# Kernel optimization log

Measured on AMD Instinct MI355X. Metric: run time of the kernel, lower is better.

## Reference

```python
import jax, jax.numpy as jnp
import numpy as np

WIDTH = 768
HEAD = 64

def setup_inputs() -> dict:
    key = jax.random.key(0)
    ks = jax.random.split(key, 8)
    x = jax.random.normal(ks[0], (8, 2048, WIDTH), dtype=jnp.float32)
    mask = jax.random.randint(ks[1], (2048, 2048), 0, 2, dtype=jnp.int32)
    s = 1.0 / np.sqrt(WIDTH)
    Wq = jax.random.normal(ks[2], (WIDTH, HEAD), dtype=jnp.float32) * s
    Wk = jax.random.normal(ks[3], (WIDTH, HEAD), dtype=jnp.float32) * s
    Wv = jax.random.normal(ks[4], (WIDTH, HEAD), dtype=jnp.float32) * s
    bq = jax.random.normal(ks[5], (HEAD,), dtype=jnp.float32) * 0.01
    bk = jax.random.normal(ks[6], (HEAD,), dtype=jnp.float32) * 0.01
    bv = jax.random.normal(ks[7], (HEAD,), dtype=jnp.float32) * 0.01
    return {"x": x, "Wq": Wq, "bq": bq, "Wk": Wk, "bk": bk, "Wv": Wv, "bv": bv, "mask": mask}

def reference(x, Wq, bq, Wk, bk, Wv, bv, mask) -> jnp.ndarray:
    # x: [B, N, width]; projections -> [B, N, head]
    Q = jnp.einsum('bnw,wh->bnh', x, Wq) + bq
    K = jnp.einsum('bnw,wh->bnh', x, Wk) + bk
    V = jnp.einsum('bnw,wh->bnh', x, Wv) + bv
    scale = 1.0 / jnp.sqrt(jnp.asarray(Q.shape[-1], dtype=Q.dtype))
    scores = jnp.einsum('bqh,bkh->bqk', Q, K) * scale  # [B, N, N]
    scores = jnp.where(mask == 0, -jnp.inf, scores)
    attn = jax.nn.softmax(scores, axis=-1)
    return jnp.einsum('bqk,bkh->bqh', attn, V)
```

## Files before the change

kernel.cpp:

```cpp
#include <hip/hip_runtime.h>

typedef short  s8v   __attribute__((ext_vector_type(8)));
typedef float  f32x4 __attribute__((ext_vector_type(4)));

#define SEQ 2048
#define WID 768

__device__ __forceinline__ unsigned fbits(float f) {
    union { float f; unsigned u; } v; v.f = f; return v.u;
}
__device__ __forceinline__ float bitsf(unsigned u) {
    union { unsigned u; float f; } v; v.u = u; return v.f;
}
__device__ __forceinline__ unsigned short f2b(float f) {
    unsigned u = fbits(f);
    return (unsigned short)((u + 0x7FFFu + ((u >> 16) & 1u)) >> 16);
}
__device__ __forceinline__ unsigned packRNE(float a, float b) {
    unsigned ta = fbits(a) + 0x7FFFu + ((fbits(a) >> 16) & 1u);
    unsigned tb = fbits(b) + 0x7FFFu + ((fbits(b) >> 16) & 1u);
    return __builtin_amdgcn_perm(tb, ta, 0x07060302u);
}
__device__ __forceinline__ unsigned packTRUNC(float a, float b) {
    return __builtin_amdgcn_perm(fbits(b), fbits(a), 0x07060302u);
}
__device__ __forceinline__ f32x4 zero4() { f32x4 z = {0.f, 0.f, 0.f, 0.f}; return z; }

__device__ __forceinline__ void async16(const unsigned short* g, void* l) {
    __builtin_amdgcn_global_load_lds(
        (const __attribute__((address_space(1))) unsigned int*)g,
        (__attribute__((address_space(3))) unsigned int*)l, 16, 0, 0);
}
__device__ __forceinline__ void async16f(const float* g, void* l) {
    __builtin_amdgcn_global_load_lds(
        (const __attribute__((address_space(1))) unsigned int*)g,
        (__attribute__((address_space(3))) unsigned int*)l, 16, 0, 0);
}
__device__ __forceinline__ void async4(const unsigned* g, void* l) {
    __builtin_amdgcn_global_load_lds(
        (const __attribute__((address_space(1))) unsigned int*)g,
        (__attribute__((address_space(3))) unsigned int*)l, 4, 0, 0);
}

__global__ __launch_bounds__(256) void convert_mask_kernel(
    const int* __restrict__ mask, unsigned* __restrict__ PM)
{
    const int tid = threadIdx.x;
    const int gid  = blockIdx.x * 4 + (tid >> 6);
    const int lane = tid & 63, quad = lane >> 4, c = lane & 15;
    const int qb = gid >> 5, kb = gid & 31;
    unsigned w = 0;
    #pragma unroll
    for (int mt = 0; mt < 2; ++mt)
        #pragma unroll
        for (int i = 0; i < 4; ++i) {
            const int q = qb * 32 + mt * 16 + quad * 4 + i;
            const int4 mm = *(const int4*)&mask[(size_t)q * SEQ + kb * 64 + 4 * c];
            if (mm.x) w |= 1u << (mt * 16 + i * 4 + 0);
            if (mm.y) w |= 1u << (mt * 16 + i * 4 + 1);
            if (mm.z) w |= 1u << (mt * 16 + i * 4 + 2);
            if (mm.w) w |= 1u << (mt * 16 + i * 4 + 3);
        }
    PM[(size_t)gid * 64 + lane] = w;
}

__global__ __launch_bounds__(256) void convert_w_kernel(
    const float* __restrict__ Wq, const float* __restrict__ Wk, const float* __restrict__ Wv,
    unsigned short* __restrict__ WF)
{
    const int s2 = blockIdx.x * 256 + threadIdx.x;
    const int chunk = s2 >> 6, l = s2 & 63;
    const int ntg = chunk / 24, r = chunk - ntg * 24;
    const int kc = r >> 1, h = r & 1;
    const int mat = ntg >> 2;
    const int col = (ntg & 3) * 16 + (l & 15);
    const int k0 = kc * 64 + h * 32 + (l >> 4) * 8;
    const float* Wm = (mat == 0) ? Wq : (mat == 1) ? Wk : Wv;
    float p[8];
    #pragma unroll
    for (int j = 0; j < 8; ++j) p[j] = Wm[(size_t)(k0 + j) * 64 + col];
    uint4 w;
    w.x = packRNE(p[0], p[1]); w.y = packRNE(p[2], p[3]);
    w.z = packRNE(p[4], p[5]); w.w = packRNE(p[6], p[7]);
    *(uint4*)&WF[(size_t)s2 * 8] = w;
}

__global__ __launch_bounds__(256, 4) void qkv_proj_kernel(
    const float* __restrict__ x, const unsigned short* __restrict__ WF,
    const float* __restrict__ bq, const float* __restrict__ bk, const float* __restrict__ bv,
    unsigned short* __restrict__ QF, unsigned short* __restrict__ KF,
    unsigned short* __restrict__ VF)
{
    __shared__ __align__(16) unsigned char SM[32768];
    unsigned short (*St)[200] = (unsigned short(*)[200])SM;

    const int tid = threadIdx.x;
    const int wv = tid >> 6, lane = tid & 63, quad = lane >> 4, c = lane & 15;
    const int cg = wv;
    const int rowb = blockIdx.x * 32;

    float bias[3];
    #pragma unroll
    for (int nt = 0; nt < 3; ++nt) {
        int col = cg * 48 + nt * 16 + c;
        const float* B = (col < 64) ? bq : (col < 128) ? bk : bv;
        bias[nt] = B[col & 63];
    }

    auto issue = [&](int kc, int b) {
        unsigned char* base = SM + b * 16384;
        #pragma unroll
        for (int r = 0; r < 4; ++r) {
            const int t = wv * 4 + r;
            if (t < 4) {
                const int mt = t >> 1, jh = t & 1;
                const float* src = x + (size_t)(rowb + mt * 16 + c) * WID
                                     + kc * 32 + quad * 8 + jh * 4;
                async16f(src, base + (mt * 2 + jh) * 1024);
            } else {
                const int i = t - 4;
                const unsigned short* src =
                    WF + (((size_t)i * 12 + (kc >> 1)) * 2 + (kc & 1)) * 512 + lane * 8;
                async16(src, base + 4096 + i * 1024);
            }
        }
    };

    f32x4 acc[2][3];
    #pragma unroll
    for (int mt = 0; mt < 2; ++mt)
        #pragma unroll
        for (int nt = 0; nt < 3; ++nt) acc[mt][nt] = zero4();

    issue(0, 0);
    for (int kc = 0; kc < 24; ++kc) {
        const int b = kc & 1;
        __syncthreads();
        if (kc < 23) issue(kc + 1, b ^ 1);

        const unsigned char* base = SM + b * 16384;
        s8v af[2];
        #pragma unroll
        for (int mt = 0; mt < 2; ++mt) {
            float4 f0 = *(const float4*)(base + (mt * 2 + 0) * 1024 + lane * 16);
            float4 f1 = *(const float4*)(base + (mt * 2 + 1) * 1024 + lane * 16);
            union { uint4 u; s8v v; } a;
            a.u.x = packRNE(f0.x, f0.y);
            a.u.y = packRNE(f0.z, f0.w);
            a.u.z = packRNE(f1.x, f1.y);
            a.u.w = packRNE(f1.z, f1.w);
            af[mt] = a.v;
        }
        s8v bf[3];
        #pragma unroll
        for (int nt = 0; nt < 3; ++nt)
            bf[nt] = *(const s8v*)(base + 4096 + (cg * 3 + nt) * 1024 + lane * 16);
        #pragma unroll
        for (int mt = 0; mt < 2; ++mt)
            #pragma unroll
            for (int nt = 0; nt < 3; ++nt)
                acc[mt][nt] = __builtin_amdgcn_mfma_f32_16x16x32_bf16(
                    af[mt], bf[nt], acc[mt][nt], 0, 0, 0);
    }

    __syncthreads();
    #pragma unroll
    for (int mt = 0; mt < 2; ++mt)
        #pragma unroll
        for (int nt = 0; nt < 3; ++nt)
            #pragma unroll
            for (int i = 0; i < 4; ++i)
                St[mt * 16 + quad * 4 + i][cg * 48 + nt * 16 + c]
                    = f2b(acc[mt][nt][i] + bias[nt]);
    __syncthreads();

    const int kb  = rowb >> 6;
    const int q0k = (rowb & 63) >> 2;
    const int ks0 = (rowb & 63) >> 5;

    {
        const int g = tid >> 7, ks = (tid >> 6) & 1, l = tid & 63;
        uint4 v = *(uint4*)&St[g * 16 + (l & 15)][ks * 32 + (l >> 4) * 8];
        *(uint4*)&QF[(((size_t)(rowb >> 4) + g) * 2 + ks) * 512 + (size_t)l * 8] = v;
    }
    {
        const int ksnt = tid >> 5, e = tid & 31;
        const int ks = ksnt >> 2, nt = ksnt & 3;
        const int qd = e >> 3, cc = e & 7;
        uint4 v = *(uint4*)&St[4 * cc + nt][64 + ks * 32 + qd * 8];
        *(uint4*)&KF[(((size_t)kb * 8 + ksnt) * 64 + qd * 16 + q0k + cc) * 8] = v;
    }
    {
        const int nt = tid >> 6, qd = (tid >> 4) & 3, cc = tid & 15;
        unsigned short p[8];
        #pragma unroll
        for (int s = 0; s < 8; ++s) p[s] = St[qd * 8 + s][128 + nt * 16 + cc];
        uint4 w;
        w.x = (unsigned)p[0] | ((unsigned)p[1] << 16);
        w.y = (unsigned)p[2] | ((unsigned)p[3] << 16);
        w.z = (unsigned)p[4] | ((unsigned)p[5] << 16);
        w.w = (unsigned)p[6] | ((unsigned)p[7] << 16);
        *(uint4*)&VF[(((size_t)kb * 8 + ks0 * 4 + nt) * 64 + qd * 16 + cc) * 8] = w;
    }
}

__global__ __launch_bounds__(512, 4) void attn_kernel(
    const unsigned short* __restrict__ QF, const unsigned short* __restrict__ KF,
    const unsigned short* __restrict__ VF, const unsigned* __restrict__ PM,
    float* __restrict__ out)
{
    __shared__ unsigned short Ks[4][4096];
    __shared__ unsigned PMs[4][64];
    __shared__ __align__(16) unsigned char PsOb[17408];
    __shared__ float Lbuf[32];
    unsigned short (*Ps)[16][68] = (unsigned short(*)[16][68])PsOb;
    float (*Obuf)[68]            = (float(*)[68])PsOb;

    const int tid = threadIdx.x;
    const int wv = tid >> 6, lane = tid & 63, quad = lane >> 4, c = lane & 15;
    const int sl = wv & 3, qh = wv >> 2;
    const int blk = blockIdx.x;
    const int bb = blk & 7, qt = blk >> 3;
    const int qrow_blk = qt * 32;

    s8v qf[2];
    {
        const size_t qgrp = (size_t)bb * 128 + qt * 2 + qh;
        #pragma unroll
        for (int ks = 0; ks < 2; ++ks)
            qf[ks] = *(const s8v*)&QF[(qgrp * 2 + ks) * 512 + (size_t)lane * 8];
    }

    f32x4 O[4];
    float lro[4];
    #pragma unroll
    for (int nt = 0; nt < 4; ++nt) O[nt] = zero4();
    #pragma unroll
    for (int i = 0; i < 4; ++i) lro[i] = 0.f;

    auto k_dma = [&](int kt) {
        const size_t kbg = (size_t)bb * 32 + sl * 8 + kt;
        #pragma unroll
        for (int r = 0; r < 4; ++r) {
            const int ch = qh * 4 + r;
            async16(KF + (kbg * 8 + ch) * 512 + lane * 8, &Ks[sl][ch * 512]);
        }
        if (qh == 0)
            async4(PM + ((size_t)qt * 32 + sl * 8 + kt) * 64 + lane, &PMs[sl][0]);
    };

    k_dma(0);
    for (int kt = 0; kt < 8; ++kt) {
        const size_t kbg = (size_t)bb * 32 + sl * 8 + kt;

        __syncthreads();

        f32x4 S[4];
        #pragma unroll
        for (int nt = 0; nt < 4; ++nt) S[nt] = zero4();
        #pragma unroll
        for (int ks = 0; ks < 2; ++ks) {
            s8v kfr[4];
            #pragma unroll
            for (int nt = 0; nt < 4; ++nt)
                kfr[nt] = *(const s8v*)&Ks[sl][((ks * 4 + nt) * 64 + lane) * 8];
            #pragma unroll
            for (int nt = 0; nt < 4; ++nt)
                S[nt] = __builtin_amdgcn_mfma_f32_16x16x32_bf16(qf[ks], kfr[nt], S[nt], 0, 0, 0);
        }

        const unsigned pmh = PMs[sl][lane] >> (qh * 16);
        #pragma unroll
        for (int i = 0; i < 4; ++i) {
            float p4[4];
            #pragma unroll
            for (int nt = 0; nt < 4; ++nt) {
                float e = exp2f(fmaf(S[nt][i], 0.18033688011112042f, -21.640425613334451f));
                p4[nt] = ((pmh >> (i * 4 + nt)) & 1u) ? e : 0.f;
            }
            unsigned u0 = packTRUNC(p4[0], p4[1]);
            unsigned u1 = packTRUNC(p4[2], p4[3]);
            lro[i] += bitsf(u0 << 16) + bitsf(u0 & 0xFFFF0000u)
                    + bitsf(u1 << 16) + bitsf(u1 & 0xFFFF0000u);
            *(uint2*)&Ps[wv][quad * 4 + i][4 * c] = make_uint2(u0, u1);
        }

        #pragma unroll
        for (int ks = 0; ks < 2; ++ks) {
            s8v vf4[4];
            #pragma unroll
            for (int nt = 0; nt < 4; ++nt)
                vf4[nt] = *(const s8v*)&VF[(kbg * 8 + ks * 4 + nt) * 512 + (size_t)lane * 8];
            s8v a = *(const s8v*)&Ps[wv][c][ks * 32 + quad * 8];
            #pragma unroll
            for (int nt = 0; nt < 4; ++nt)
                O[nt] = __builtin_amdgcn_mfma_f32_16x16x32_bf16(a, vf4[nt], O[nt], 0, 0, 0);
        }

        __syncthreads();
        if (kt < 7) k_dma(kt + 1);
    }

    __syncthreads();
    #pragma unroll
    for (int j = 0; j < 5; ++j) {
        int idx = tid + 512 * j;
        if (idx < 32 * 68) ((float*)Obuf)[idx] = 0.f;
    }
    if (tid < 32) Lbuf[tid] = 0.f;
    __syncthreads();
    #pragma unroll
    for (int i = 0; i < 4; ++i) {
        float l = lro[i];
        l += __shfl_xor(l, 1);
        l += __shfl_xor(l, 2);
        l += __shfl_xor(l, 4);
        l += __shfl_xor(l, 8);
        if (c == 0) atomicAdd(&Lbuf[qh * 16 + quad * 4 + i], l);
        #pragma unroll
        for (int nt = 0; nt < 4; ++nt)
            atomicAdd(&Obuf[qh * 16 + quad * 4 + i][nt * 16 + c], O[nt][i]);
    }
    __syncthreads();
    {
        const int r = tid >> 4, d4 = (tid & 15) * 4;
        const float invL = 1.0f / Lbuf[r];
        float4 v = *(float4*)&Obuf[r][d4];
        float4 o = make_float4(v.x * invL, v.y * invL, v.z * invL, v.w * invL);
        *(float4*)&out[((size_t)bb * SEQ + qrow_blk + r) * 64 + d4] = o;
    }
}

extern "C" void kernel_launch(void* const* d_in, const int* in_sizes, int n_in,
                              void* d_out, int out_size, void* d_ws, size_t ws_size,
                              hipStream_t stream)
{
    const float* x    = (const float*)d_in[0];
    const float* Wq   = (const float*)d_in[1];
    const float* bq   = (const float*)d_in[2];
    const float* Wk   = (const float*)d_in[3];
    const float* bk   = (const float*)d_in[4];
    const float* Wv   = (const float*)d_in[5];
    const float* bv   = (const float*)d_in[6];
    const int*   mask = (const int*)d_in[7];
    float* out = (float*)d_out;

    unsigned short* QF = (unsigned short*)d_ws;
    unsigned short* KF = QF + (size_t)16384 * 64;
    unsigned short* VF = KF + (size_t)16384 * 64;
    unsigned short* WF = VF + (size_t)16384 * 64;
    unsigned*       PM = (unsigned*)(WF + (size_t)192 * WID);

    convert_mask_kernel<<<512, 256, 0, stream>>>(mask, PM);
    convert_w_kernel<<<72, 256, 0, stream>>>(Wq, Wk, Wv, WF);
    qkv_proj_kernel<<<512, 256, 0, stream>>>(x, WF, bq, bk, bv, QF, KF, VF);
    attn_kernel<<<512, 512, 0, stream>>>(QF, KF, VF, PM, out);
}
```

Baseline: 174.0 us.

## Fuse convert kernels, widen QKV k-chunks, double-buffer K tiles in 64-row attention blocks

Merges the mask and weight conversion kernels into one launch. Doubles the per-stage k-chunk in the QKV projection, halving its barrier count at the cost of more shared memory and a lower occupancy bound. Restructures attention into 1024-thread blocks covering 64 query rows, with double-buffered K/mask DMA so the next tile loads while the current one is computed, removing a barrier per iteration. The larger blocks halve the grid and raise shared-memory use per block.

```diff
diff --git a/kernel.cpp b/kernel.cpp
--- a/kernel.cpp
+++ b/kernel.cpp
@@ -42,56 +42,56 @@
         (__attribute__((address_space(3))) unsigned int*)l, 4, 0, 0);
 }
 
-__global__ __launch_bounds__(256) void convert_mask_kernel(
-    const int* __restrict__ mask, unsigned* __restrict__ PM)
+__global__ __launch_bounds__(256) void convert_kernel(
+    const int* __restrict__ mask,
+    const float* __restrict__ Wq, const float* __restrict__ Wk, const float* __restrict__ Wv,
+    unsigned* __restrict__ PM, unsigned short* __restrict__ WF)
 {
     const int tid = threadIdx.x;
-    const int gid  = blockIdx.x * 4 + (tid >> 6);
-    const int lane = tid & 63, quad = lane >> 4, c = lane & 15;
-    const int qb = gid >> 5, kb = gid & 31;
-    unsigned w = 0;
-    #pragma unroll
-    for (int mt = 0; mt < 2; ++mt)
-        #pragma unroll
-        for (int i = 0; i < 4; ++i) {
-            const int q = qb * 32 + mt * 16 + quad * 4 + i;
-            const int4 mm = *(const int4*)&mask[(size_t)q * SEQ + kb * 64 + 4 * c];
-            if (mm.x) w |= 1u << (mt * 16 + i * 4 + 0);
-            if (mm.y) w |= 1u << (mt * 16 + i * 4 + 1);
-            if (mm.z) w |= 1u << (mt * 16 + i * 4 + 2);
-            if (mm.w) w |= 1u << (mt * 16 + i * 4 + 3);
-        }
-    PM[(size_t)gid * 64 + lane] = w;
-}
-
-__global__ __launch_bounds__(256) void convert_w_kernel(
-    const float* __restrict__ Wq, const float* __restrict__ Wk, const float* __restrict__ Wv,
-    unsigned short* __restrict__ WF)
-{
-    const int s2 = blockIdx.x * 256 + threadIdx.x;
-    const int chunk = s2 >> 6, l = s2 & 63;
-    const int ntg = chunk / 24, r = chunk - ntg * 24;
-    const int kc = r >> 1, h = r & 1;
-    const int mat = ntg >> 2;
-    const int col = (ntg & 3) * 16 + (l & 15);
-    const int k0 = kc * 64 + h * 32 + (l >> 4) * 8;
-    const float* Wm = (mat == 0) ? Wq : (mat == 1) ? Wk : Wv;
-    float p[8];
-    #pragma unroll
-    for (int j = 0; j < 8; ++j) p[j] = Wm[(size_t)(k0 + j) * 64 + col];
-    uint4 w;
-    w.x = packRNE(p[0], p[1]); w.y = packRNE(p[2], p[3]);
-    w.z = packRNE(p[4], p[5]); w.w = packRNE(p[6], p[7]);
-    *(uint4*)&WF[(size_t)s2 * 8] = w;
-}
-
-__global__ __launch_bounds__(256, 4) void qkv_proj_kernel(
+    const int blk = blockIdx.x;
+    if (blk < 512) {
+        const int gid  = blk * 4 + (tid >> 6);
+        const int lane = tid & 63, quad = lane >> 4, c = lane & 15;
+        const int qb = gid >> 5, kb = gid & 31;
+        unsigned w = 0;
+        #pragma unroll
+        for (int mt = 0; mt < 2; ++mt)
+            #pragma unroll
+            for (int i = 0; i < 4; ++i) {
+                const int q = qb * 32 + mt * 16 + quad * 4 + i;
+                const int4 mm = *(const int4*)&mask[(size_t)q * SEQ + kb * 64 + 4 * c];
+                if (mm.x) w |= 1u << (mt * 16 + i * 4 + 0);
+                if (mm.y) w |= 1u << (mt * 16 + i * 4 + 1);
+                if (mm.z) w |= 1u << (mt * 16 + i * 4 + 2);
+                if (mm.w) w |= 1u << (mt * 16 + i * 4 + 3);
+            }
+        PM[(size_t)gid * 64 + lane] = w;
+    } else {
+        const int s2 = (blk - 512) * 256 + tid;
+        const int chunk = s2 >> 6, l = s2 & 63;
+        const int ntg = chunk / 24, r = chunk - ntg * 24;
+        const int kc = r >> 1, h = r & 1;
+        const int mat = ntg >> 2;
+        const int col = (ntg & 3) * 16 + (l & 15);
+        const int k0 = kc * 64 + h * 32 + (l >> 4) * 8;
+        const float* Wm = (mat == 0) ? Wq : (mat == 1) ? Wk : Wv;
+        float p[8];
+        #pragma unroll
+        for (int j = 0; j < 8; ++j) p[j] = Wm[(size_t)(k0 + j) * 64 + col];
+        uint4 w;
+        w.x = packRNE(p[0], p[1]); w.y = packRNE(p[2], p[3]);
+        w.z = packRNE(p[4], p[5]); w.w = packRNE(p[6], p[7]);
+        *(uint4*)&WF[(size_t)s2 * 8] = w;
+    }
+}
+
+__global__ __launch_bounds__(256, 2) void qkv_proj_kernel(
     const float* __restrict__ x, const unsigned short* __restrict__ WF,
     const float* __restrict__ bq, const float* __restrict__ bk, const float* __restrict__ bv,
     unsigned short* __restrict__ QF, unsigned short* __restrict__ KF,
     unsigned short* __restrict__ VF)
 {
-    __shared__ __align__(16) unsigned char SM[32768];
+    __shared__ __align__(16) unsigned char SM[65536];
     unsigned short (*St)[200] = (unsigned short(*)[200])SM;
 
     const int tid = threadIdx.x;
@@ -108,20 +108,20 @@
     }
 
     auto issue = [&](int kc, int b) {
-        unsigned char* base = SM + b * 16384;
-        #pragma unroll
-        for (int r = 0; r < 4; ++r) {
-            const int t = wv * 4 + r;
-            if (t < 4) {
-                const int mt = t >> 1, jh = t & 1;
-                const float* src = x + (size_t)(rowb + mt * 16 + c) * WID
-                                     + kc * 32 + quad * 8 + jh * 4;
-                async16f(src, base + (mt * 2 + jh) * 1024);
+        unsigned char* base = SM + b * 32768;
+        #pragma unroll
+        for (int r = 0; r < 8; ++r) {
+            const int t = wv * 8 + r;
+            if (t < 8) {
+                const int g = t >> 2, kh = (t >> 1) & 1, jh = t & 1;
+                const float* src = x + (size_t)(rowb + g * 16 + c) * WID
+                                     + kc * 64 + kh * 32 + quad * 8 + jh * 4;
+                async16f(src, base + t * 1024);
             } else {
-                const int i = t - 4;
+                const int i = t - 8, ntg = i >> 1, kh = i & 1;
                 const unsigned short* src =
-                    WF + (((size_t)i * 12 + (kc >> 1)) * 2 + (kc & 1)) * 512 + lane * 8;
-                async16(src, base + 4096 + i * 1024);
+                    WF + (((size_t)ntg * 12 + kc) * 2 + kh) * 512 + lane * 8;
+                async16(src, base + 8192 + i * 1024);
             }
         }
     };
@@ -133,34 +133,37 @@
         for (int nt = 0; nt < 3; ++nt) acc[mt][nt] = zero4();
 
     issue(0, 0);
-    for (int kc = 0; kc < 24; ++kc) {
+    for (int kc = 0; kc < 12; ++kc) {
         const int b = kc & 1;
         __syncthreads();
-        if (kc < 23) issue(kc + 1, b ^ 1);
-
-        const unsigned char* base = SM + b * 16384;
-        s8v af[2];
-        #pragma unroll
-        for (int mt = 0; mt < 2; ++mt) {
-            float4 f0 = *(const float4*)(base + (mt * 2 + 0) * 1024 + lane * 16);
-            float4 f1 = *(const float4*)(base + (mt * 2 + 1) * 1024 + lane * 16);
-            union { uint4 u; s8v v; } a;
-            a.u.x = packRNE(f0.x, f0.y);
-            a.u.y = packRNE(f0.z, f0.w);
-            a.u.z = packRNE(f1.x, f1.y);
-            a.u.w = packRNE(f1.z, f1.w);
-            af[mt] = a.v;
-        }
-        s8v bf[3];
-        #pragma unroll
-        for (int nt = 0; nt < 3; ++nt)
-            bf[nt] = *(const s8v*)(base + 4096 + (cg * 3 + nt) * 1024 + lane * 16);
-        #pragma unroll
-        for (int mt = 0; mt < 2; ++mt)
+        if (kc < 11) issue(kc + 1, b ^ 1);
+
+        const unsigned char* base = SM + b * 32768;
+        #pragma unroll
+        for (int kh = 0; kh < 2; ++kh) {
+            s8v af[2];
+            #pragma unroll
+            for (int mt = 0; mt < 2; ++mt) {
+                float4 f0 = *(const float4*)(base + (mt * 4 + kh * 2 + 0) * 1024 + lane * 16);
+                float4 f1 = *(const float4*)(base + (mt * 4 + kh * 2 + 1) * 1024 + lane * 16);
+                union { uint4 u; s8v v; } a;
+                a.u.x = packRNE(f0.x, f0.y);
+                a.u.y = packRNE(f0.z, f0.w);
+                a.u.z = packRNE(f1.x, f1.y);
+                a.u.w = packRNE(f1.z, f1.w);
+                af[mt] = a.v;
+            }
+            s8v bf[3];
             #pragma unroll
             for (int nt = 0; nt < 3; ++nt)
-                acc[mt][nt] = __builtin_amdgcn_mfma_f32_16x16x32_bf16(
-                    af[mt], bf[nt], acc[mt][nt], 0, 0, 0);
+                bf[nt] = *(const s8v*)(base + 8192 + ((cg * 3 + nt) * 2 + kh) * 1024 + lane * 16);
+            #pragma unroll
+            for (int mt = 0; mt < 2; ++mt)
+                #pragma unroll
+                for (int nt = 0; nt < 3; ++nt)
+                    acc[mt][nt] = __builtin_amdgcn_mfma_f32_16x16x32_bf16(
+                        af[mt], bf[nt], acc[mt][nt], 0, 0, 0);
+        }
     }
 
     __syncthreads();
@@ -204,28 +207,27 @@
     }
 }
 
-__global__ __launch_bounds__(512, 4) void attn_kernel(
+__global__ __launch_bounds__(1024, 4) void attn_kernel(
     const unsigned short* __restrict__ QF, const unsigned short* __restrict__ KF,
     const unsigned short* __restrict__ VF, const unsigned* __restrict__ PM,
     float* __restrict__ out)
 {
-    __shared__ unsigned short Ks[4][4096];
-    __shared__ unsigned PMs[4][64];
-    __shared__ __align__(16) unsigned char PsOb[17408];
-    __shared__ float Lbuf[32];
+    __shared__ unsigned short Ks[2][4][4096];
+    __shared__ unsigned PMs[2][2][4][64];
+    __shared__ __align__(16) unsigned char PsOb[34816];
+    __shared__ float Lbuf[64];
     unsigned short (*Ps)[16][68] = (unsigned short(*)[16][68])PsOb;
     float (*Obuf)[68]            = (float(*)[68])PsOb;
 
     const int tid = threadIdx.x;
     const int wv = tid >> 6, lane = tid & 63, quad = lane >> 4, c = lane & 15;
-    const int sl = wv & 3, qh = wv >> 2;
+    const int sl = wv & 3, qg = wv >> 2, mt = qg & 1;
     const int blk = blockIdx.x;
     const int bb = blk & 7, qt = blk >> 3;
-    const int qrow_blk = qt * 32;
 
     s8v qf[2];
     {
-        const size_t qgrp = (size_t)bb * 128 + qt * 2 + qh;
+        const size_t qgrp = (size_t)bb * 128 + qt * 4 + qg;
         #pragma unroll
         for (int ks = 0; ks < 2; ++ks)
             qf[ks] = *(const s8v*)&QF[(qgrp * 2 + ks) * 512 + (size_t)lane * 8];
@@ -238,22 +240,28 @@
     #pragma unroll
     for (int i = 0; i < 4; ++i) lro[i] = 0.f;
 
-    auto k_dma = [&](int kt) {
+    auto dma = [&](int kt, int b) {
         const size_t kbg = (size_t)bb * 32 + sl * 8 + kt;
         #pragma unroll
-        for (int r = 0; r < 4; ++r) {
-            const int ch = qh * 4 + r;
-            async16(KF + (kbg * 8 + ch) * 512 + lane * 8, &Ks[sl][ch * 512]);
-        }
-        if (qh == 0)
-            async4(PM + ((size_t)qt * 32 + sl * 8 + kt) * 64 + lane, &PMs[sl][0]);
+        for (int r = 0; r < 2; ++r) {
+            const int ch = qg * 2 + r;
+            async16(KF + (kbg * 8 + ch) * 512 + lane * 8, &Ks[b][sl][ch * 512]);
+        }
+        if (qg == 0)
+            async4(PM + ((size_t)(qt * 2 + 0) * 32 + sl * 8 + kt) * 64 + lane,
+                   &PMs[b][0][sl][0]);
+        if (qg == 2)
+            async4(PM + ((size_t)(qt * 2 + 1) * 32 + sl * 8 + kt) * 64 + lane,
+                   &PMs[b][1][sl][0]);
     };
 
-    k_dma(0);
+    dma(0, 0);
     for (int kt = 0; kt < 8; ++kt) {
+        const int b = kt & 1;
+        __syncthreads();
+        if (kt < 7) dma(kt + 1, b ^ 1);
+
         const size_t kbg = (size_t)bb * 32 + sl * 8 + kt;
-
-        __syncthreads();
 
         f32x4 S[4];
         #pragma unroll
@@ -263,13 +271,13 @@
             s8v kfr[4];
             #pragma unroll
             for (int nt = 0; nt < 4; ++nt)
-                kfr[nt] = *(const s8v*)&Ks[sl][((ks * 4 + nt) * 64 + lane) * 8];
+                kfr[nt] = *(const s8v*)&Ks[b][sl][((ks * 4 + nt) * 64 + lane) * 8];
             #pragma unroll
             for (int nt = 0; nt < 4; ++nt)
                 S[nt] = __builtin_amdgcn_mfma_f32_16x16x32_bf16(qf[ks], kfr[nt], S[nt], 0, 0, 0);
         }
 
-        const unsigned pmh = PMs[sl][lane] >> (qh * 16);
+        const unsigned pmh = PMs[b][qg >> 1][sl][lane] >> (mt * 16);
         #pragma unroll
         for (int i = 0; i < 4; ++i) {
             float p4[4];
@@ -296,18 +304,15 @@
             for (int nt = 0; nt < 4; ++nt)
                 O[nt] = __builtin_amdgcn_mfma_f32_16x16x32_bf16(a, vf4[nt], O[nt], 0, 0, 0);
         }
-
-        __syncthreads();
-        if (kt < 7) k_dma(kt + 1);
     }
 
     __syncthreads();
     #pragma unroll
     for (int j = 0; j < 5; ++j) {
-        int idx = tid + 512 * j;
-        if (idx < 32 * 68) ((float*)Obuf)[idx] = 0.f;
-    }
-    if (tid < 32) Lbuf[tid] = 0.f;
+        int idx = tid + 1024 * j;
+        if (idx < 64 * 68) ((float*)Obuf)[idx] = 0.f;
+    }
+    if (tid < 64) Lbuf[tid] = 0.f;
     __syncthreads();
     #pragma unroll
     for (int i = 0; i < 4; ++i) {
@@ -316,10 +321,10 @@
         l += __shfl_xor(l, 2);
         l += __shfl_xor(l, 4);
         l += __shfl_xor(l, 8);
-        if (c == 0) atomicAdd(&Lbuf[qh * 16 + quad * 4 + i], l);
+        if (c == 0) atomicAdd(&Lbuf[qg * 16 + quad * 4 + i], l);
         #pragma unroll
         for (int nt = 0; nt < 4; ++nt)
-            atomicAdd(&Obuf[qh * 16 + quad * 4 + i][nt * 16 + c], O[nt][i]);
+            atomicAdd(&Obuf[qg * 16 + quad * 4 + i][nt * 16 + c], O[nt][i]);
     }
     __syncthreads();
     {
@@ -327,7 +332,7 @@
         const float invL = 1.0f / Lbuf[r];
         float4 v = *(float4*)&Obuf[r][d4];
         float4 o = make_float4(v.x * invL, v.y * invL, v.z * invL, v.w * invL);
-        *(float4*)&out[((size_t)bb * SEQ + qrow_blk + r) * 64 + d4] = o;
+        *(float4*)&out[((size_t)bb * SEQ + qt * 64 + r) * 64 + d4] = o;
     }
 }
 
@@ -351,8 +356,7 @@
     unsigned short* WF = VF + (size_t)16384 * 64;
     unsigned*       PM = (unsigned*)(WF + (size_t)192 * WID);
 
-    convert_mask_kernel<<<512, 256, 0, stream>>>(mask, PM);
-    convert_w_kernel<<<72, 256, 0, stream>>>(Wq, Wk, Wv, WF);
+    convert_kernel<<<584, 256, 0, stream>>>(mask, Wq, Wk, Wv, PM, WF);
     qkv_proj_kernel<<<512, 256, 0, stream>>>(x, WF, bq, bk, bv, QF, KF, VF);
-    attn_kernel<<<512, 512, 0, stream>>>(QF, KF, VF, PM, out);
-}
+    attn_kernel<<<256, 1024, 0, stream>>>(QF, KF, VF, PM, out);
+}
```

Result: faster. 164.3 us (-5.6%).
